# Kernel optimization log

Measured on AMD Instinct MI355X. Metric: run time of the kernel, lower is better.

The kernel has to match this reference:

```python
import jax, jax.numpy as jnp
import numpy as np

N_EMBD = 1024
HEADS = 16
HEAD_DIM = N_EMBD // HEADS


def setup_inputs() -> dict:
    key = jax.random.key(0)
    k1, k2 = jax.random.split(key)
    x = jax.random.normal(k1, (2, 2048, N_EMBD), dtype=jnp.float32)
    W_qkv = jax.random.normal(k2, (N_EMBD, 3 * N_EMBD), dtype=jnp.float32) * (N_EMBD ** -0.5)
    b_qkv = jnp.zeros((3 * N_EMBD,), dtype=jnp.float32)
    return {"x": x, "W_qkv": W_qkv, "b_qkv": b_qkv}


def reference(x, W_qkv, b_qkv):
    B, T, _ = x.shape
    qkv = x @ W_qkv + b_qkv                      # [B, T, 3*n_embd]
    q, k, v = jnp.split(qkv, 3, axis=-1)
    q = q.reshape(B, T, HEADS, HEAD_DIM)
    k = k.reshape(B, T, HEADS, HEAD_DIM)
    v = v.reshape(B, T, HEADS, HEAD_DIM)
    attn = jnp.einsum('bthd,bThd->bhtT', q, k) / jnp.sqrt(jnp.float32(HEAD_DIM))
    causal = jnp.tril(jnp.ones((T, T), dtype=bool))  # [T, T]
    attn = jnp.where(causal, attn, -jnp.inf)
    attn = jax.nn.softmax(attn, axis=-1)
    # dropout is identity in deterministic/eval mode (training=False)
    out = jnp.einsum('bhtT,bThd->bthd', attn, v).reshape(B, T, N_EMBD)
    return out
```

## Files before the change

### kernel.cpp

```cpp
#include <hip/hip_runtime.h>
#include <hip/hip_bf16.h>

#define BATCH 2
#define TSEQ  2048
#define NEMBD 1024
#define HEADS 16
#define HDIM  64

typedef short          bf16x8 __attribute__((ext_vector_type(8)));
typedef float          f32x4  __attribute__((ext_vector_type(4)));
typedef unsigned short u16;

__device__ __forceinline__ u16 f2bf(float f) {
  unsigned int u = __float_as_uint(f);
  u += 0x7fffu + ((u >> 16) & 1u);
  return (u16)(u >> 16);
}

__device__ __forceinline__ void gld16(const u16* g, u16* l) {
  __builtin_amdgcn_global_load_lds(
      (const __attribute__((address_space(1))) unsigned int*)g,
      (__attribute__((address_space(3))) unsigned int*)l, 16, 0, 0);
}

__global__ __launch_bounds__(256) void k_convert_x(const float* __restrict__ x,
                                                   u16* __restrict__ xb) {
  int i = blockIdx.x * 256 + threadIdx.x;
  float4 v = ((const float4*)x)[i];
  ushort4 o;
  o.x = f2bf(v.x); o.y = f2bf(v.y); o.z = f2bf(v.z); o.w = f2bf(v.w);
  ((ushort4*)xb)[i] = o;
}

__global__ __launch_bounds__(256) void k_transpose_w(const float* __restrict__ w,
                                                     u16* __restrict__ wt) {
  __shared__ float tile[32][33];
  const int n0 = blockIdx.x * 32;
  const int k0 = blockIdx.y * 32;
  const int t  = threadIdx.x;
  const int r  = t >> 3;
  const int c4 = (t & 7) * 4;
  float4 v = *(const float4*)(w + (size_t)(k0 + r) * 3072 + n0 + c4);
  tile[r][c4 + 0] = v.x; tile[r][c4 + 1] = v.y;
  tile[r][c4 + 2] = v.z; tile[r][c4 + 3] = v.w;
  __syncthreads();
  ushort4 o;
  o.x = f2bf(tile[c4 + 0][r]);
  o.y = f2bf(tile[c4 + 1][r]);
  o.z = f2bf(tile[c4 + 2][r]);
  o.w = f2bf(tile[c4 + 3][r]);
  *(ushort4*)(wt + (size_t)(n0 + r) * 1024 + k0 + c4) = o;
}

__global__ __launch_bounds__(256, 3) void k_qkv_gemm(
    const u16* __restrict__ xb, const u16* __restrict__ wt,
    const float* __restrict__ bias,
    u16* __restrict__ qb, u16* __restrict__ kbuf, u16* __restrict__ vt) {
  __shared__ u16 As[128 * 32];
  __shared__ u16 Bs[128 * 32];

  const int t    = threadIdx.x;
  const int wv   = t >> 6;
  const int lane = t & 63;
  const int m    = lane & 15;
  const int quad = lane >> 4;
  const int lin  = blockIdx.x;
  const int cp   = lin >> 5;
  const int rp   = ((lin & 7) << 2) | ((lin >> 3) & 3);
  const int row0 = rp * 128;
  const int col0 = cp * 128;
  const int wr   = (wv >> 1) * 64;
  const int wc   = (wv & 1) * 64;

  const int srow = wv * 32 + (lane >> 2);
  const int scol = (lane & 3) * 8;
  const u16* ag = xb + (size_t)(row0 + srow) * 1024 + scol;
  const u16* bg = wt + (size_t)(col0 + srow) * 1024 + scol;
  u16* al = As + (wv * 32) * 32;
  u16* bl = Bs + (wv * 32) * 32;

  f32x4 acc[4][4];
  const f32x4 zf = {0.f, 0.f, 0.f, 0.f};
  for (int i = 0; i < 4; ++i)
    for (int j = 0; j < 4; ++j) acc[i][j] = zf;

  for (int kt = 0; kt < 32; ++kt) {
    const int kk = kt * 32;
    __syncthreads();
    gld16(ag + kk,             al);
    gld16(ag + kk + 16 * 1024, al + 16 * 32);
    gld16(bg + kk,             bl);
    gld16(bg + kk + 16 * 1024, bl + 16 * 32);
    __syncthreads();

    bf16x8 af[4], bfr[4];
#pragma unroll
    for (int mt = 0; mt < 4; ++mt)
      af[mt] = *(const bf16x8*)(As + (wr + mt * 16 + m) * 32 + quad * 8);
#pragma unroll
    for (int nt = 0; nt < 4; ++nt)
      bfr[nt] = *(const bf16x8*)(Bs + (wc + nt * 16 + m) * 32 + quad * 8);
#pragma unroll
    for (int mt = 0; mt < 4; ++mt)
#pragma unroll
      for (int nt = 0; nt < 4; ++nt)
        acc[mt][nt] = __builtin_amdgcn_mfma_f32_16x16x32_bf16(
            af[mt], bfr[nt], acc[mt][nt], 0, 0, 0);
  }

  const int sec = col0 >> 10;
#pragma unroll
  for (int nt = 0; nt < 4; ++nt) {
    const int Cc = col0 + wc + nt * 16 + m;
    const float bv = bias[Cc];
    const int c = Cc & 1023;
    const int h = c >> 6;
    const int d = c & 63;
#pragma unroll
    for (int mt = 0; mt < 4; ++mt) {
      const int Rbase = row0 + wr + mt * 16 + quad * 4;
      const int bb = Rbase >> 11;
      const int t0 = Rbase & 2047;
      const int bh = bb * HEADS + h;
      if (sec == 0) {
#pragma unroll
        for (int rg = 0; rg < 4; ++rg) {
          float v = (acc[mt][nt][rg] + bv) * 0.125f;
          qb[(size_t)(bh * TSEQ + t0 + rg) * HDIM + d] = f2bf(v);
        }
      } else if (sec == 1) {
#pragma unroll
        for (int rg = 0; rg < 4; ++rg) {
          float v = acc[mt][nt][rg] + bv;
          kbuf[(size_t)(bh * TSEQ + t0 + rg) * HDIM + d] = f2bf(v);
        }
      } else {
        ushort4 pk;
        pk.x = f2bf(acc[mt][nt][0] + bv);
        pk.y = f2bf(acc[mt][nt][1] + bv);
        pk.z = f2bf(acc[mt][nt][2] + bv);
        pk.w = f2bf(acc[mt][nt][3] + bv);
        *(ushort4*)(vt + (size_t)(bh * HDIM + d) * TSEQ + t0) = pk;
      }
    }
  }
}

__global__ __launch_bounds__(256, 3) void k_attn(
    const u16* __restrict__ qb, const u16* __restrict__ kbuf,
    const u16* __restrict__ vt, float* __restrict__ out) {
  __shared__ __align__(16) u16 Kb[2][4096];
  __shared__ __align__(16) u16 Vb[2][4096];
  __shared__ __align__(16) u16 pt[4][16 * 72];

  const int t     = threadIdx.x;
  const int wv    = t >> 6;
  const int lane  = t & 63;
  const int m     = lane & 15;
  const int quad  = lane >> 4;
  const int bh    = blockIdx.x & 31;
  const int qtg   = 31 - (blockIdx.x >> 5);
  const int qbase = (qtg * 4 + wv) * 16;
  const int nkt   = qtg + 1;

  u16* pw = &pt[wv][0];

  const u16* qrow = qb + ((size_t)bh * TSEQ + qbase + m) * HDIM + quad * 8;
  bf16x8 aq0 = *(const bf16x8*)(qrow);
  bf16x8 aq1 = *(const bf16x8*)(qrow + 32);

  const int sr = wv * 16 + (lane >> 3);
  const int gs = (lane & 7) ^ (sr & 7);
  const u16* kg = kbuf + ((size_t)bh * TSEQ + sr) * HDIM + gs * 8;
  const u16* vg = vt + ((size_t)bh * HDIM + sr) * TSEQ + gs * 8;
  u16* klds = &Kb[0][wv * 16 * 64];
  u16* vlds = &Vb[0][wv * 16 * 64];

  const int swL = (quad ^ (m & 7)) * 8;
  const int swH = ((quad + 4) ^ (m & 7)) * 8;

  f32x4 o[4];
  const f32x4 zf = {0.f, 0.f, 0.f, 0.f};
  for (int nt = 0; nt < 4; ++nt) o[nt] = zf;
  float rsum = 0.f;
  const int qi = qbase + m;

  gld16(kg,             klds);
  gld16(kg + 8 * HDIM,  klds + 8 * 64);
  gld16(vg,             vlds);
  gld16(vg + 8 * TSEQ,  vlds + 8 * 64);
  __syncthreads();

  for (int kt = 0; kt < nkt; ++kt) {
    const int b = kt & 1;
    const u16* kb0 = &Kb[b][0];
    const u16* vb0 = &Vb[b][0];

    f32x4 s[4];
    for (int nt = 0; nt < 4; ++nt) s[nt] = zf;
#pragma unroll
    for (int nt = 0; nt < 4; ++nt) {
      bf16x8 kf = *(const bf16x8*)(kb0 + (nt * 16 + m) * 64 + swL);
      s[nt] = __builtin_amdgcn_mfma_f32_16x16x32_bf16(kf, aq0, s[nt], 0, 0, 0);
    }
#pragma unroll
    for (int nt = 0; nt < 4; ++nt) {
      bf16x8 kf = *(const bf16x8*)(kb0 + (nt * 16 + m) * 64 + swH);
      s[nt] = __builtin_amdgcn_mfma_f32_16x16x32_bf16(kf, aq1, s[nt], 0, 0, 0);
    }

    bf16x8 vfL[4], vfH[4];
#pragma unroll
    for (int nt = 0; nt < 4; ++nt) {
      vfL[nt] = *(const bf16x8*)(vb0 + (nt * 16 + m) * 64 + swL);
      vfH[nt] = *(const bf16x8*)(vb0 + (nt * 16 + m) * 64 + swH);
    }

    if (kt + 1 < nkt) {
      const int nb = (kt + 1) & 1;
      const u16* kgn = kg + (size_t)(kt + 1) * 64 * HDIM;
      const u16* vgn = vg + (kt + 1) * 64;
      u16* kl = &Kb[nb][wv * 16 * 64];
      u16* vl = &Vb[nb][wv * 16 * 64];
      gld16(kgn,            kl);
      gld16(kgn + 8 * HDIM, kl + 8 * 64);
      gld16(vgn,            vl);
      gld16(vgn + 8 * TSEQ, vl + 8 * 64);
    }

    if (kt == nkt - 1) {
      const int kb = kt * 64 + quad * 4;
#pragma unroll
      for (int nt = 0; nt < 4; ++nt)
#pragma unroll
        for (int rg = 0; rg < 4; ++rg)
          if (kb + nt * 16 + rg > qi) s[nt][rg] = -1e30f;
    }

#pragma unroll
    for (int nt = 0; nt < 4; ++nt) {
      float p0 = __expf(s[nt][0]), p1 = __expf(s[nt][1]);
      float p2 = __expf(s[nt][2]), p3 = __expf(s[nt][3]);
      rsum += (p0 + p1) + (p2 + p3);
      ushort4 pk = {f2bf(p0), f2bf(p1), f2bf(p2), f2bf(p3)};
      *(ushort4*)(pw + m * 72 + nt * 16 + quad * 4) = pk;
    }
    bf16x8 bp0 = *(const bf16x8*)(pw + m * 72 + quad * 8);
    bf16x8 bp1 = *(const bf16x8*)(pw + m * 72 + 32 + quad * 8);

#pragma unroll
    for (int nt = 0; nt < 4; ++nt)
      o[nt] = __builtin_amdgcn_mfma_f32_16x16x32_bf16(vfL[nt], bp0, o[nt], 0, 0, 0);
#pragma unroll
    for (int nt = 0; nt < 4; ++nt)
      o[nt] = __builtin_amdgcn_mfma_f32_16x16x32_bf16(vfH[nt], bp1, o[nt], 0, 0, 0);

    __syncthreads();
  }

  rsum += __shfl_xor(rsum, 16);
  rsum += __shfl_xor(rsum, 32);
  const float inv = 1.0f / rsum;

  const int bb = bh >> 4;
  const int h  = bh & 15;
  float* ob = out + ((size_t)(bb * TSEQ + qi) * NEMBD + h * HDIM + quad * 4);
#pragma unroll
  for (int nt = 0; nt < 4; ++nt) {
    float4 st;
    st.x = o[nt][0] * inv; st.y = o[nt][1] * inv;
    st.z = o[nt][2] * inv; st.w = o[nt][3] * inv;
    *(float4*)(ob + nt * 16) = st;
  }
}

extern "C" void kernel_launch(void* const* d_in, const int* in_sizes, int n_in,
                              void* d_out, int out_size, void* d_ws, size_t ws_size,
                              hipStream_t stream) {
  (void)in_sizes; (void)n_in; (void)out_size; (void)ws_size;
  const float* x    = (const float*)d_in[0];
  const float* W    = (const float*)d_in[1];
  const float* bqkv = (const float*)d_in[2];
  float* out = (float*)d_out;

  u16* ws   = (u16*)d_ws;
  u16* qb   = ws;
  u16* kbuf = ws + 4194304;
  u16* vt   = ws + 2 * 4194304;
  u16* xb   = ws + 3 * 4194304;
  u16* wt   = ws + 4 * 4194304;

  hipLaunchKernelGGL(k_convert_x, dim3(4096), dim3(256), 0, stream, x, xb);
  hipLaunchKernelGGL(k_transpose_w, dim3(96, 32), dim3(256), 0, stream, W, wt);
  hipLaunchKernelGGL(k_qkv_gemm, dim3(768), dim3(256), 0, stream,
                     xb, wt, bqkv, qb, kbuf, vt);
  hipLaunchKernelGGL(k_attn, dim3(1024), dim3(256), 0, stream,
                     qb, kbuf, vt, out);
}
```

Before: 143.5 us.

## Fuse prep kernels, double-buffer GEMM LDS, process two query tiles per attention wave

The x conversion and the W transpose now run as a single launch, which removes one kernel launch. The QKV GEMM double-buffers its LDS tiles so that global loads for the next k-step overlap the MFMAs of the current one. It also drops one barrier per iteration. Attention waves now handle 32 query rows instead of 16, so K/V fragments loaded from LDS are reused twice and the grid is halved, at the cost of more registers, higher LDS use and fewer blocks to balance the causal load.

```diff
diff --git a/kernel.cpp b/kernel.cpp
--- a/kernel.cpp
+++ b/kernel.cpp
@@ -23,21 +23,23 @@
       (__attribute__((address_space(3))) unsigned int*)l, 16, 0, 0);
 }
 
-__global__ __launch_bounds__(256) void k_convert_x(const float* __restrict__ x,
-                                                   u16* __restrict__ xb) {
-  int i = blockIdx.x * 256 + threadIdx.x;
-  float4 v = ((const float4*)x)[i];
-  ushort4 o;
-  o.x = f2bf(v.x); o.y = f2bf(v.y); o.z = f2bf(v.z); o.w = f2bf(v.w);
-  ((ushort4*)xb)[i] = o;
-}
-
-__global__ __launch_bounds__(256) void k_transpose_w(const float* __restrict__ w,
-                                                     u16* __restrict__ wt) {
+__global__ __launch_bounds__(256) void k_prep(const float* __restrict__ x,
+                                              u16* __restrict__ xb,
+                                              const float* __restrict__ w,
+                                              u16* __restrict__ wt) {
   __shared__ float tile[32][33];
-  const int n0 = blockIdx.x * 32;
-  const int k0 = blockIdx.y * 32;
-  const int t  = threadIdx.x;
+  const int t = threadIdx.x;
+  if (blockIdx.x < 4096) {
+    int i = blockIdx.x * 256 + t;
+    float4 v = ((const float4*)x)[i];
+    ushort4 o;
+    o.x = f2bf(v.x); o.y = f2bf(v.y); o.z = f2bf(v.z); o.w = f2bf(v.w);
+    ((ushort4*)xb)[i] = o;
+    return;
+  }
+  const int bid = blockIdx.x - 4096;
+  const int n0 = (bid % 96) * 32;
+  const int k0 = (bid / 96) * 32;
   const int r  = t >> 3;
   const int c4 = (t & 7) * 4;
   float4 v = *(const float4*)(w + (size_t)(k0 + r) * 3072 + n0 + c4);
@@ -56,8 +58,8 @@
     const u16* __restrict__ xb, const u16* __restrict__ wt,
     const float* __restrict__ bias,
     u16* __restrict__ qb, u16* __restrict__ kbuf, u16* __restrict__ vt) {
-  __shared__ u16 As[128 * 32];
-  __shared__ u16 Bs[128 * 32];
+  __shared__ u16 As[2][128 * 32];
+  __shared__ u16 Bs[2][128 * 32];
 
   const int t    = threadIdx.x;
   const int wv   = t >> 6;
@@ -76,36 +78,50 @@
   const int scol = (lane & 3) * 8;
   const u16* ag = xb + (size_t)(row0 + srow) * 1024 + scol;
   const u16* bg = wt + (size_t)(col0 + srow) * 1024 + scol;
-  u16* al = As + (wv * 32) * 32;
-  u16* bl = Bs + (wv * 32) * 32;
+  u16* al[2] = {&As[0][(wv * 32) * 32], &As[1][(wv * 32) * 32]};
+  u16* bl[2] = {&Bs[0][(wv * 32) * 32], &Bs[1][(wv * 32) * 32]};
 
   f32x4 acc[4][4];
   const f32x4 zf = {0.f, 0.f, 0.f, 0.f};
   for (int i = 0; i < 4; ++i)
     for (int j = 0; j < 4; ++j) acc[i][j] = zf;
 
+  gld16(ag,             al[0]);
+  gld16(ag + 16 * 1024, al[0] + 16 * 32);
+  gld16(bg,             bl[0]);
+  gld16(bg + 16 * 1024, bl[0] + 16 * 32);
+  __syncthreads();
+
   for (int kt = 0; kt < 32; ++kt) {
-    const int kk = kt * 32;
-    __syncthreads();
-    gld16(ag + kk,             al);
-    gld16(ag + kk + 16 * 1024, al + 16 * 32);
-    gld16(bg + kk,             bl);
-    gld16(bg + kk + 16 * 1024, bl + 16 * 32);
-    __syncthreads();
+    const int b = kt & 1;
+    const u16* Ab = &As[b][0];
+    const u16* Bb = &Bs[b][0];
 
     bf16x8 af[4], bfr[4];
 #pragma unroll
     for (int mt = 0; mt < 4; ++mt)
-      af[mt] = *(const bf16x8*)(As + (wr + mt * 16 + m) * 32 + quad * 8);
+      af[mt] = *(const bf16x8*)(Ab + (wr + mt * 16 + m) * 32 + quad * 8);
 #pragma unroll
     for (int nt = 0; nt < 4; ++nt)
-      bfr[nt] = *(const bf16x8*)(Bs + (wc + nt * 16 + m) * 32 + quad * 8);
+      bfr[nt] = *(const bf16x8*)(Bb + (wc + nt * 16 + m) * 32 + quad * 8);
+
+    if (kt + 1 < 32) {
+      const int kk = (kt + 1) * 32;
+      const int nb = b ^ 1;
+      gld16(ag + kk,             al[nb]);
+      gld16(ag + kk + 16 * 1024, al[nb] + 16 * 32);
+      gld16(bg + kk,             bl[nb]);
+      gld16(bg + kk + 16 * 1024, bl[nb] + 16 * 32);
+    }
+
 #pragma unroll
     for (int mt = 0; mt < 4; ++mt)
 #pragma unroll
       for (int nt = 0; nt < 4; ++nt)
         acc[mt][nt] = __builtin_amdgcn_mfma_f32_16x16x32_bf16(
             af[mt], bfr[nt], acc[mt][nt], 0, 0, 0);
+
+    __syncthreads();
   }
 
   const int sec = col0 >> 10;
@@ -151,7 +167,7 @@
     const u16* __restrict__ vt, float* __restrict__ out) {
   __shared__ __align__(16) u16 Kb[2][4096];
   __shared__ __align__(16) u16 Vb[2][4096];
-  __shared__ __align__(16) u16 pt[4][16 * 72];
+  __shared__ __align__(16) u16 pt[4][2][16 * 72];
 
   const int t     = threadIdx.x;
   const int wv    = t >> 6;
@@ -159,36 +175,44 @@
   const int m     = lane & 15;
   const int quad  = lane >> 4;
   const int bh    = blockIdx.x & 31;
-  const int qtg   = 31 - (blockIdx.x >> 5);
-  const int qbase = (qtg * 4 + wv) * 16;
-  const int nkt   = qtg + 1;
-
-  u16* pw = &pt[wv][0];
-
-  const u16* qrow = qb + ((size_t)bh * TSEQ + qbase + m) * HDIM + quad * 8;
-  bf16x8 aq0 = *(const bf16x8*)(qrow);
-  bf16x8 aq1 = *(const bf16x8*)(qrow + 32);
+  const int j     = blockIdx.x >> 5;
+  const int g     = (j < 8) ? (15 - j) : (j - 8);
+  const int qb0   = g * 128 + wv * 32;
+  const int nkt   = 2 * g + 2;
+  const int diag0 = qb0 >> 6;
+  const int diag1 = (qb0 + 16) >> 6;
+
+  u16* pw0 = &pt[wv][0][0];
+  u16* pw1 = &pt[wv][1][0];
+
+  const u16* qr0 = qb + ((size_t)bh * TSEQ + qb0 + m) * HDIM + quad * 8;
+  const u16* qr1 = qr0 + 16 * HDIM;
+  bf16x8 aq00 = *(const bf16x8*)(qr0);
+  bf16x8 aq01 = *(const bf16x8*)(qr0 + 32);
+  bf16x8 aq10 = *(const bf16x8*)(qr1);
+  bf16x8 aq11 = *(const bf16x8*)(qr1 + 32);
 
   const int sr = wv * 16 + (lane >> 3);
   const int gs = (lane & 7) ^ (sr & 7);
   const u16* kg = kbuf + ((size_t)bh * TSEQ + sr) * HDIM + gs * 8;
   const u16* vg = vt + ((size_t)bh * HDIM + sr) * TSEQ + gs * 8;
-  u16* klds = &Kb[0][wv * 16 * 64];
-  u16* vlds = &Vb[0][wv * 16 * 64];
+  u16* klds[2] = {&Kb[0][wv * 16 * 64], &Kb[1][wv * 16 * 64]};
+  u16* vlds[2] = {&Vb[0][wv * 16 * 64], &Vb[1][wv * 16 * 64]};
 
   const int swL = (quad ^ (m & 7)) * 8;
   const int swH = ((quad + 4) ^ (m & 7)) * 8;
 
-  f32x4 o[4];
+  f32x4 o0[4], o1[4];
   const f32x4 zf = {0.f, 0.f, 0.f, 0.f};
-  for (int nt = 0; nt < 4; ++nt) o[nt] = zf;
-  float rsum = 0.f;
-  const int qi = qbase + m;
-
-  gld16(kg,             klds);
-  gld16(kg + 8 * HDIM,  klds + 8 * 64);
-  gld16(vg,             vlds);
-  gld16(vg + 8 * TSEQ,  vlds + 8 * 64);
+  for (int nt = 0; nt < 4; ++nt) { o0[nt] = zf; o1[nt] = zf; }
+  float r0 = 0.f, r1 = 0.f;
+  const int qi0 = qb0 + m;
+  const int qi1 = qb0 + 16 + m;
+
+  gld16(kg,            klds[0]);
+  gld16(kg + 8 * HDIM, klds[0] + 8 * 64);
+  gld16(vg,            vlds[0]);
+  gld16(vg + 8 * TSEQ, vlds[0] + 8 * 64);
   __syncthreads();
 
   for (int kt = 0; kt < nkt; ++kt) {
@@ -196,81 +220,116 @@
     const u16* kb0 = &Kb[b][0];
     const u16* vb0 = &Vb[b][0];
 
-    f32x4 s[4];
-    for (int nt = 0; nt < 4; ++nt) s[nt] = zf;
+    bf16x8 kf[8], vfL[4], vfH[4];
 #pragma unroll
     for (int nt = 0; nt < 4; ++nt) {
-      bf16x8 kf = *(const bf16x8*)(kb0 + (nt * 16 + m) * 64 + swL);
-      s[nt] = __builtin_amdgcn_mfma_f32_16x16x32_bf16(kf, aq0, s[nt], 0, 0, 0);
-    }
-#pragma unroll
-    for (int nt = 0; nt < 4; ++nt) {
-      bf16x8 kf = *(const bf16x8*)(kb0 + (nt * 16 + m) * 64 + swH);
-      s[nt] = __builtin_amdgcn_mfma_f32_16x16x32_bf16(kf, aq1, s[nt], 0, 0, 0);
-    }
-
-    bf16x8 vfL[4], vfH[4];
-#pragma unroll
-    for (int nt = 0; nt < 4; ++nt) {
-      vfL[nt] = *(const bf16x8*)(vb0 + (nt * 16 + m) * 64 + swL);
-      vfH[nt] = *(const bf16x8*)(vb0 + (nt * 16 + m) * 64 + swH);
+      kf[nt]     = *(const bf16x8*)(kb0 + (nt * 16 + m) * 64 + swL);
+      kf[nt + 4] = *(const bf16x8*)(kb0 + (nt * 16 + m) * 64 + swH);
+      vfL[nt]    = *(const bf16x8*)(vb0 + (nt * 16 + m) * 64 + swL);
+      vfH[nt]    = *(const bf16x8*)(vb0 + (nt * 16 + m) * 64 + swH);
     }
 
     if (kt + 1 < nkt) {
       const int nb = (kt + 1) & 1;
       const u16* kgn = kg + (size_t)(kt + 1) * 64 * HDIM;
       const u16* vgn = vg + (kt + 1) * 64;
-      u16* kl = &Kb[nb][wv * 16 * 64];
-      u16* vl = &Vb[nb][wv * 16 * 64];
-      gld16(kgn,            kl);
-      gld16(kgn + 8 * HDIM, kl + 8 * 64);
-      gld16(vgn,            vl);
-      gld16(vgn + 8 * TSEQ, vl + 8 * 64);
-    }
-
-    if (kt == nkt - 1) {
-      const int kb = kt * 64 + quad * 4;
-#pragma unroll
-      for (int nt = 0; nt < 4; ++nt)
-#pragma unroll
-        for (int rg = 0; rg < 4; ++rg)
-          if (kb + nt * 16 + rg > qi) s[nt][rg] = -1e30f;
-    }
-
-#pragma unroll
-    for (int nt = 0; nt < 4; ++nt) {
-      float p0 = __expf(s[nt][0]), p1 = __expf(s[nt][1]);
-      float p2 = __expf(s[nt][2]), p3 = __expf(s[nt][3]);
-      rsum += (p0 + p1) + (p2 + p3);
-      ushort4 pk = {f2bf(p0), f2bf(p1), f2bf(p2), f2bf(p3)};
-      *(ushort4*)(pw + m * 72 + nt * 16 + quad * 4) = pk;
-    }
-    bf16x8 bp0 = *(const bf16x8*)(pw + m * 72 + quad * 8);
-    bf16x8 bp1 = *(const bf16x8*)(pw + m * 72 + 32 + quad * 8);
-
-#pragma unroll
-    for (int nt = 0; nt < 4; ++nt)
-      o[nt] = __builtin_amdgcn_mfma_f32_16x16x32_bf16(vfL[nt], bp0, o[nt], 0, 0, 0);
-#pragma unroll
-    for (int nt = 0; nt < 4; ++nt)
-      o[nt] = __builtin_amdgcn_mfma_f32_16x16x32_bf16(vfH[nt], bp1, o[nt], 0, 0, 0);
+      gld16(kgn,            klds[nb]);
+      gld16(kgn + 8 * HDIM, klds[nb] + 8 * 64);
+      gld16(vgn,            vlds[nb]);
+      gld16(vgn + 8 * TSEQ, vlds[nb] + 8 * 64);
+    }
+
+    const int kbq = kt * 64 + quad * 4;
+
+    {
+      f32x4 s[4];
+      for (int nt = 0; nt < 4; ++nt) s[nt] = zf;
+#pragma unroll
+      for (int nt = 0; nt < 4; ++nt)
+        s[nt] = __builtin_amdgcn_mfma_f32_16x16x32_bf16(kf[nt], aq00, s[nt], 0, 0, 0);
+#pragma unroll
+      for (int nt = 0; nt < 4; ++nt)
+        s[nt] = __builtin_amdgcn_mfma_f32_16x16x32_bf16(kf[nt + 4], aq01, s[nt], 0, 0, 0);
+      if (kt >= diag0) {
+#pragma unroll
+        for (int nt = 0; nt < 4; ++nt)
+#pragma unroll
+          for (int rg = 0; rg < 4; ++rg)
+            if (kbq + nt * 16 + rg > qi0) s[nt][rg] = -1e30f;
+      }
+#pragma unroll
+      for (int nt = 0; nt < 4; ++nt) {
+        float p0 = __expf(s[nt][0]), p1 = __expf(s[nt][1]);
+        float p2 = __expf(s[nt][2]), p3 = __expf(s[nt][3]);
+        r0 += (p0 + p1) + (p2 + p3);
+        ushort4 pk = {f2bf(p0), f2bf(p1), f2bf(p2), f2bf(p3)};
+        *(ushort4*)(pw0 + m * 72 + nt * 16 + quad * 4) = pk;
+      }
+      bf16x8 bp0 = *(const bf16x8*)(pw0 + m * 72 + quad * 8);
+      bf16x8 bp1 = *(const bf16x8*)(pw0 + m * 72 + 32 + quad * 8);
+#pragma unroll
+      for (int nt = 0; nt < 4; ++nt)
+        o0[nt] = __builtin_amdgcn_mfma_f32_16x16x32_bf16(vfL[nt], bp0, o0[nt], 0, 0, 0);
+#pragma unroll
+      for (int nt = 0; nt < 4; ++nt)
+        o0[nt] = __builtin_amdgcn_mfma_f32_16x16x32_bf16(vfH[nt], bp1, o0[nt], 0, 0, 0);
+    }
+
+    {
+      f32x4 s[4];
+      for (int nt = 0; nt < 4; ++nt) s[nt] = zf;
+#pragma unroll
+      for (int nt = 0; nt < 4; ++nt)
+        s[nt] = __builtin_amdgcn_mfma_f32_16x16x32_bf16(kf[nt], aq10, s[nt], 0, 0, 0);
+#pragma unroll
+      for (int nt = 0; nt < 4; ++nt)
+        s[nt] = __builtin_amdgcn_mfma_f32_16x16x32_bf16(kf[nt + 4], aq11, s[nt], 0, 0, 0);
+      if (kt >= diag1) {
+#pragma unroll
+        for (int nt = 0; nt < 4; ++nt)
+#pragma unroll
+          for (int rg = 0; rg < 4; ++rg)
+            if (kbq + nt * 16 + rg > qi1) s[nt][rg] = -1e30f;
+      }
+#pragma unroll
+      for (int nt = 0; nt < 4; ++nt) {
+        float p0 = __expf(s[nt][0]), p1 = __expf(s[nt][1]);
+        float p2 = __expf(s[nt][2]), p3 = __expf(s[nt][3]);
+        r1 += (p0 + p1) + (p2 + p3);
+        ushort4 pk = {f2bf(p0), f2bf(p1), f2bf(p2), f2bf(p3)};
+        *(ushort4*)(pw1 + m * 72 + nt * 16 + quad * 4) = pk;
+      }
+      bf16x8 bp0 = *(const bf16x8*)(pw1 + m * 72 + quad * 8);
+      bf16x8 bp1 = *(const bf16x8*)(pw1 + m * 72 + 32 + quad * 8);
+#pragma unroll
+      for (int nt = 0; nt < 4; ++nt)
+        o1[nt] = __builtin_amdgcn_mfma_f32_16x16x32_bf16(vfL[nt], bp0, o1[nt], 0, 0, 0);
+#pragma unroll
+      for (int nt = 0; nt < 4; ++nt)
+        o1[nt] = __builtin_amdgcn_mfma_f32_16x16x32_bf16(vfH[nt], bp1, o1[nt], 0, 0, 0);
+    }
 
     __syncthreads();
   }
 
-  rsum += __shfl_xor(rsum, 16);
-  rsum += __shfl_xor(rsum, 32);
-  const float inv = 1.0f / rsum;
+  r0 += __shfl_xor(r0, 16); r0 += __shfl_xor(r0, 32);
+  r1 += __shfl_xor(r1, 16); r1 += __shfl_xor(r1, 32);
+  const float inv0 = 1.0f / r0;
+  const float inv1 = 1.0f / r1;
 
   const int bb = bh >> 4;
   const int h  = bh & 15;
-  float* ob = out + ((size_t)(bb * TSEQ + qi) * NEMBD + h * HDIM + quad * 4);
+  float* ob0 = out + ((size_t)(bb * TSEQ + qi0) * NEMBD + h * HDIM + quad * 4);
+  float* ob1 = out + ((size_t)(bb * TSEQ + qi1) * NEMBD + h * HDIM + quad * 4);
 #pragma unroll
   for (int nt = 0; nt < 4; ++nt) {
-    float4 st;
-    st.x = o[nt][0] * inv; st.y = o[nt][1] * inv;
-    st.z = o[nt][2] * inv; st.w = o[nt][3] * inv;
-    *(float4*)(ob + nt * 16) = st;
+    float4 s0, s1;
+    s0.x = o0[nt][0] * inv0; s0.y = o0[nt][1] * inv0;
+    s0.z = o0[nt][2] * inv0; s0.w = o0[nt][3] * inv0;
+    *(float4*)(ob0 + nt * 16) = s0;
+    s1.x = o1[nt][0] * inv1; s1.y = o1[nt][1] * inv1;
+    s1.z = o1[nt][2] * inv1; s1.w = o1[nt][3] * inv1;
+    *(float4*)(ob1 + nt * 16) = s1;
   }
 }
 
@@ -290,10 +349,9 @@
   u16* xb   = ws + 3 * 4194304;
   u16* wt   = ws + 4 * 4194304;
 
-  hipLaunchKernelGGL(k_convert_x, dim3(4096), dim3(256), 0, stream, x, xb);
-  hipLaunchKernelGGL(k_transpose_w, dim3(96, 32), dim3(256), 0, stream, W, wt);
+  hipLaunchKernelGGL(k_prep, dim3(7168), dim3(256), 0, stream, x, xb, W, wt);
   hipLaunchKernelGGL(k_qkv_gemm, dim3(768), dim3(256), 0, stream,
                      xb, wt, bqkv, qb, kbuf, vt);
-  hipLaunchKernelGGL(k_attn, dim3(1024), dim3(256), 0, stream,
+  hipLaunchKernelGGL(k_attn, dim3(512), dim3(256), 0, stream,
                      qb, kbuf, vt, out);
 }
```

After: 173.9 us. +21.2%, slower.

## Merge prep kernels, double-buffer QKV GEMM, swizzle P tile, raise attn occupancy

Applied to the files above, without the earlier changes.

Folds the x conversion and W transpose into a single launch, which removes one kernel launch. Double-buffers the QKV GEMM's LDS tiles so the next K-slice loads while MFMAs run, leaving one barrier per iteration instead of two. In attention, the probability tile moves from padded rows to an XOR-swizzled 64-wide layout to avoid LDS bank conflicts and save shared memory. Attention launch bounds also rise from 3 to 4 waves per SIMD, which may force register spills, and the doubled GEMM LDS may lower its occupancy.

```diff
diff --git a/kernel.cpp b/kernel.cpp
--- a/kernel.cpp
+++ b/kernel.cpp
@@ -23,21 +23,23 @@
       (__attribute__((address_space(3))) unsigned int*)l, 16, 0, 0);
 }
 
-__global__ __launch_bounds__(256) void k_convert_x(const float* __restrict__ x,
-                                                   u16* __restrict__ xb) {
-  int i = blockIdx.x * 256 + threadIdx.x;
-  float4 v = ((const float4*)x)[i];
-  ushort4 o;
-  o.x = f2bf(v.x); o.y = f2bf(v.y); o.z = f2bf(v.z); o.w = f2bf(v.w);
-  ((ushort4*)xb)[i] = o;
-}
-
-__global__ __launch_bounds__(256) void k_transpose_w(const float* __restrict__ w,
-                                                     u16* __restrict__ wt) {
+__global__ __launch_bounds__(256) void k_prep(const float* __restrict__ x,
+                                              u16* __restrict__ xb,
+                                              const float* __restrict__ w,
+                                              u16* __restrict__ wt) {
   __shared__ float tile[32][33];
-  const int n0 = blockIdx.x * 32;
-  const int k0 = blockIdx.y * 32;
-  const int t  = threadIdx.x;
+  const int t = threadIdx.x;
+  if (blockIdx.x < 4096) {
+    int i = blockIdx.x * 256 + t;
+    float4 v = ((const float4*)x)[i];
+    ushort4 o;
+    o.x = f2bf(v.x); o.y = f2bf(v.y); o.z = f2bf(v.z); o.w = f2bf(v.w);
+    ((ushort4*)xb)[i] = o;
+    return;
+  }
+  const int bid = blockIdx.x - 4096;
+  const int n0 = (bid % 96) * 32;
+  const int k0 = (bid / 96) * 32;
   const int r  = t >> 3;
   const int c4 = (t & 7) * 4;
   float4 v = *(const float4*)(w + (size_t)(k0 + r) * 3072 + n0 + c4);
@@ -56,8 +58,8 @@
     const u16* __restrict__ xb, const u16* __restrict__ wt,
     const float* __restrict__ bias,
     u16* __restrict__ qb, u16* __restrict__ kbuf, u16* __restrict__ vt) {
-  __shared__ u16 As[128 * 32];
-  __shared__ u16 Bs[128 * 32];
+  __shared__ u16 As[2][128 * 32];
+  __shared__ u16 Bs[2][128 * 32];
 
   const int t    = threadIdx.x;
   const int wv   = t >> 6;
@@ -76,36 +78,50 @@
   const int scol = (lane & 3) * 8;
   const u16* ag = xb + (size_t)(row0 + srow) * 1024 + scol;
   const u16* bg = wt + (size_t)(col0 + srow) * 1024 + scol;
-  u16* al = As + (wv * 32) * 32;
-  u16* bl = Bs + (wv * 32) * 32;
+  u16* al[2] = {&As[0][(wv * 32) * 32], &As[1][(wv * 32) * 32]};
+  u16* bl[2] = {&Bs[0][(wv * 32) * 32], &Bs[1][(wv * 32) * 32]};
 
   f32x4 acc[4][4];
   const f32x4 zf = {0.f, 0.f, 0.f, 0.f};
   for (int i = 0; i < 4; ++i)
     for (int j = 0; j < 4; ++j) acc[i][j] = zf;
 
+  gld16(ag,             al[0]);
+  gld16(ag + 16 * 1024, al[0] + 16 * 32);
+  gld16(bg,             bl[0]);
+  gld16(bg + 16 * 1024, bl[0] + 16 * 32);
+  __syncthreads();
+
   for (int kt = 0; kt < 32; ++kt) {
-    const int kk = kt * 32;
-    __syncthreads();
-    gld16(ag + kk,             al);
-    gld16(ag + kk + 16 * 1024, al + 16 * 32);
-    gld16(bg + kk,             bl);
-    gld16(bg + kk + 16 * 1024, bl + 16 * 32);
-    __syncthreads();
+    const int b = kt & 1;
+    const u16* Ab = &As[b][0];
+    const u16* Bb = &Bs[b][0];
 
     bf16x8 af[4], bfr[4];
 #pragma unroll
     for (int mt = 0; mt < 4; ++mt)
-      af[mt] = *(const bf16x8*)(As + (wr + mt * 16 + m) * 32 + quad * 8);
+      af[mt] = *(const bf16x8*)(Ab + (wr + mt * 16 + m) * 32 + quad * 8);
 #pragma unroll
     for (int nt = 0; nt < 4; ++nt)
-      bfr[nt] = *(const bf16x8*)(Bs + (wc + nt * 16 + m) * 32 + quad * 8);
+      bfr[nt] = *(const bf16x8*)(Bb + (wc + nt * 16 + m) * 32 + quad * 8);
+
+    if (kt + 1 < 32) {
+      const int kk = (kt + 1) * 32;
+      const int nb = b ^ 1;
+      gld16(ag + kk,             al[nb]);
+      gld16(ag + kk + 16 * 1024, al[nb] + 16 * 32);
+      gld16(bg + kk,             bl[nb]);
+      gld16(bg + kk + 16 * 1024, bl[nb] + 16 * 32);
+    }
+
 #pragma unroll
     for (int mt = 0; mt < 4; ++mt)
 #pragma unroll
       for (int nt = 0; nt < 4; ++nt)
         acc[mt][nt] = __builtin_amdgcn_mfma_f32_16x16x32_bf16(
             af[mt], bfr[nt], acc[mt][nt], 0, 0, 0);
+
+    __syncthreads();
   }
 
   const int sec = col0 >> 10;
@@ -146,12 +162,12 @@
   }
 }
 
-__global__ __launch_bounds__(256, 3) void k_attn(
+__global__ __launch_bounds__(256, 4) void k_attn(
     const u16* __restrict__ qb, const u16* __restrict__ kbuf,
     const u16* __restrict__ vt, float* __restrict__ out) {
   __shared__ __align__(16) u16 Kb[2][4096];
   __shared__ __align__(16) u16 Vb[2][4096];
-  __shared__ __align__(16) u16 pt[4][16 * 72];
+  __shared__ __align__(16) u16 pt[4][1024];
 
   const int t     = threadIdx.x;
   const int wv    = t >> 6;
@@ -164,6 +180,7 @@
   const int nkt   = qtg + 1;
 
   u16* pw = &pt[wv][0];
+  const int mm = m & 7;
 
   const u16* qrow = qb + ((size_t)bh * TSEQ + qbase + m) * HDIM + quad * 8;
   bf16x8 aq0 = *(const bf16x8*)(qrow);
@@ -173,11 +190,11 @@
   const int gs = (lane & 7) ^ (sr & 7);
   const u16* kg = kbuf + ((size_t)bh * TSEQ + sr) * HDIM + gs * 8;
   const u16* vg = vt + ((size_t)bh * HDIM + sr) * TSEQ + gs * 8;
-  u16* klds = &Kb[0][wv * 16 * 64];
-  u16* vlds = &Vb[0][wv * 16 * 64];
-
-  const int swL = (quad ^ (m & 7)) * 8;
-  const int swH = ((quad + 4) ^ (m & 7)) * 8;
+  u16* klds[2] = {&Kb[0][wv * 16 * 64], &Kb[1][wv * 16 * 64]};
+  u16* vlds[2] = {&Vb[0][wv * 16 * 64], &Vb[1][wv * 16 * 64]};
+
+  const int swL = (quad ^ mm) * 8;
+  const int swH = ((quad + 4) ^ mm) * 8;
 
   f32x4 o[4];
   const f32x4 zf = {0.f, 0.f, 0.f, 0.f};
@@ -185,10 +202,10 @@
   float rsum = 0.f;
   const int qi = qbase + m;
 
-  gld16(kg,             klds);
-  gld16(kg + 8 * HDIM,  klds + 8 * 64);
-  gld16(vg,             vlds);
-  gld16(vg + 8 * TSEQ,  vlds + 8 * 64);
+  gld16(kg,            klds[0]);
+  gld16(kg + 8 * HDIM, klds[0] + 8 * 64);
+  gld16(vg,            vlds[0]);
+  gld16(vg + 8 * TSEQ, vlds[0] + 8 * 64);
   __syncthreads();
 
   for (int kt = 0; kt < nkt; ++kt) {
@@ -220,12 +237,10 @@
       const int nb = (kt + 1) & 1;
       const u16* kgn = kg + (size_t)(kt + 1) * 64 * HDIM;
       const u16* vgn = vg + (kt + 1) * 64;
-      u16* kl = &Kb[nb][wv * 16 * 64];
-      u16* vl = &Vb[nb][wv * 16 * 64];
-      gld16(kgn,            kl);
-      gld16(kgn + 8 * HDIM, kl + 8 * 64);
-      gld16(vgn,            vl);
-      gld16(vgn + 8 * TSEQ, vl + 8 * 64);
+      gld16(kgn,            klds[nb]);
+      gld16(kgn + 8 * HDIM, klds[nb] + 8 * 64);
+      gld16(vgn,            vlds[nb]);
+      gld16(vgn + 8 * TSEQ, vlds[nb] + 8 * 64);
     }
 
     if (kt == nkt - 1) {
@@ -243,10 +258,11 @@
       float p2 = __expf(s[nt][2]), p3 = __expf(s[nt][3]);
       rsum += (p0 + p1) + (p2 + p3);
       ushort4 pk = {f2bf(p0), f2bf(p1), f2bf(p2), f2bf(p3)};
-      *(ushort4*)(pw + m * 72 + nt * 16 + quad * 4) = pk;
-    }
-    bf16x8 bp0 = *(const bf16x8*)(pw + m * 72 + quad * 8);
-    bf16x8 bp1 = *(const bf16x8*)(pw + m * 72 + 32 + quad * 8);
+      *(ushort4*)(pw + m * 64 + (((2 * nt + (quad >> 1)) ^ mm) * 8)
+                  + (quad & 1) * 4) = pk;
+    }
+    bf16x8 bp0 = *(const bf16x8*)(pw + m * 64 + swL);
+    bf16x8 bp1 = *(const bf16x8*)(pw + m * 64 + swH);
 
 #pragma unroll
     for (int nt = 0; nt < 4; ++nt)
@@ -290,8 +306,7 @@
   u16* xb   = ws + 3 * 4194304;
   u16* wt   = ws + 4 * 4194304;
 
-  hipLaunchKernelGGL(k_convert_x, dim3(4096), dim3(256), 0, stream, x, xb);
-  hipLaunchKernelGGL(k_transpose_w, dim3(96, 32), dim3(256), 0, stream, W, wt);
+  hipLaunchKernelGGL(k_prep, dim3(7168), dim3(256), 0, stream, x, xb, W, wt);
   hipLaunchKernelGGL(k_qkv_gemm, dim3(768), dim3(256), 0, stream,
                      xb, wt, bqkv, qb, kbuf, vt);
   hipLaunchKernelGGL(k_attn, dim3(1024), dim3(256), 0, stream,
```

New measurement: 145.0 us. Within noise of the previous version (+1.1%).
